# Performance work log

Hardware: AMD Instinct MI355X
Metric: run time of the kernel (lower is better)

The kernel has to match this reference:

```python
import jax, jax.numpy as jnp
import numpy as np

B, N, DIN, H, A = 4096, 32, 256, 128, 32  # batch, n_agents, din, hidden_dim, n_actions
NEG = 9e15


def _linear_params(key, fan_in, fan_out):
    kw, kb = jax.random.split(key)
    bound = 1.0 / np.sqrt(fan_in)
    w = jax.random.uniform(kw, (fan_in, fan_out), jnp.float32, -bound, bound)
    b = jax.random.uniform(kb, (fan_out,), jnp.float32, -bound, bound)
    return w, b


def setup_inputs() -> dict:
    key = jax.random.key(0)
    ks = jax.random.split(key, 12)
    x = jax.random.normal(ks[0], (B, N, DIN), jnp.float32)
    mask = jax.random.randint(ks[1], (B, N, N), 0, 2).astype(jnp.float32)
    enc_w, enc_b = _linear_params(ks[2], DIN, H)
    a1_vw, a1_vb = _linear_params(ks[3], H, H)
    a1_kw, a1_kb = _linear_params(ks[4], H, H)
    a1_qw, a1_qb = _linear_params(ks[5], H, H)
    a1_ow, a1_ob = _linear_params(ks[6], H, H)
    a2_vw, a2_vb = _linear_params(ks[7], H, H)
    a2_kw, a2_kb = _linear_params(ks[8], H, H)
    a2_qw, a2_qb = _linear_params(ks[9], H, H)
    a2_ow, a2_ob = _linear_params(ks[10], H, H)
    q_w, q_b = _linear_params(ks[11], H, A)
    return dict(x=x, mask=mask, enc_w=enc_w, enc_b=enc_b,
                a1_vw=a1_vw, a1_vb=a1_vb, a1_kw=a1_kw, a1_kb=a1_kb,
                a1_qw=a1_qw, a1_qb=a1_qb, a1_ow=a1_ow, a1_ob=a1_ob,
                a2_vw=a2_vw, a2_vb=a2_vb, a2_kw=a2_kw, a2_kb=a2_kb,
                a2_qw=a2_qw, a2_qb=a2_qb, a2_ow=a2_ow, a2_ob=a2_ob,
                q_w=q_w, q_b=q_b)


def _att_block(h, mask, vw, vb, kw, kb, qw, qb, ow, ob):
    # h: [B, N, H]; mask: [B, N, N]
    v = jax.nn.relu(jnp.einsum('bnd,dh->bnh', h, vw) + vb)
    q = jax.nn.relu(jnp.einsum('bnd,dh->bnh', h, qw) + qb)
    k = jax.nn.relu(jnp.einsum('bnd,dh->bnh', h, kw) + kb)
    scores = jnp.einsum('bih,bjh->bij', q, k)               # [B, N, N]
    logits = scores * mask - NEG * (1.0 - mask)
    att = jax.nn.softmax(logits, axis=2)
    out = jnp.einsum('bij,bjh->bih', att, v)
    return jax.nn.relu(jnp.einsum('bnh,ho->bno', out, ow) + ob)


def reference(x, mask, enc_w, enc_b,
              a1_vw, a1_vb, a1_kw, a1_kb, a1_qw, a1_qb, a1_ow, a1_ob,
              a2_vw, a2_vb, a2_kw, a2_kb, a2_qw, a2_qb, a2_ow, a2_ob,
              q_w, q_b):
    h1 = jax.nn.relu(jnp.einsum('bnd,dh->bnh', x, enc_w) + enc_b)
    h2 = _att_block(h1, mask, a1_vw, a1_vb, a1_kw, a1_kb, a1_qw, a1_qb, a1_ow, a1_ob)
    h3 = _att_block(h2, mask, a2_vw, a2_vb, a2_kw, a2_kb, a2_qw, a2_qb, a2_ow, a2_ob)
    q = jnp.einsum('bnh,ha->bna', h3, q_w) + q_b            # [B, N, A]
    return q
```

## Files before the change

kernel.cpp:

```cpp
#include <hip/hip_runtime.h>
#include <hip/hip_bf16.h>

typedef __attribute__((ext_vector_type(8))) short bf16x8;
typedef __attribute__((ext_vector_type(4))) short bf16x4;
typedef __attribute__((ext_vector_type(4))) float f32x4;

#define DEVI static __device__ __forceinline__

constexpr int NAG = 32, DIN = 256, HDIM = 128, ADIM = 32;

constexpr int WS_ENC = 0;
constexpr int WS_H   = 32768;
constexpr int WS_QW  = 32768 + 8 * 16384;
constexpr int WS_TOT = WS_QW + 4096;

constexpr int SH = 136;
constexpr int SV = 40;
constexpr int SA = 40;
constexpr int SX = 264;

constexpr int L_P0 = 0;
constexpr int L_P1 = 8704;
constexpr int L_P2 = 17408;
constexpr int L_PV = 26112;
constexpr int L_TOT = 36352;

DEVI short f2bf(float f) {
  union { float f; unsigned u; } a; a.f = f;
  return (short)((a.u + 0x7fffu + ((a.u >> 16) & 1u)) >> 16);
}

__global__ void prep_weights(const float* __restrict__ enc_w,
                             const float* __restrict__ m0, const float* __restrict__ m1,
                             const float* __restrict__ m2, const float* __restrict__ m3,
                             const float* __restrict__ m4, const float* __restrict__ m5,
                             const float* __restrict__ m6, const float* __restrict__ m7,
                             const float* __restrict__ qw,
                             short* __restrict__ ws)
{
  const int blk = blockIdx.x, tid = threadIdx.x;
  const float* src; int base, NM, nsh, f4;
  if (blk < 32) { src = enc_w; base = WS_ENC; NM = 8; nsh = 7; f4 = blk * 256 + tid; }
  else if (blk < 160) {
    const int m = (blk - 32) >> 4;
    if      (m == 0) src = m0; else if (m == 1) src = m1;
    else if (m == 2) src = m2; else if (m == 3) src = m3;
    else if (m == 4) src = m4; else if (m == 5) src = m5;
    else if (m == 6) src = m6; else             src = m7;
    base = WS_H + (m << 14); NM = 8; nsh = 7; f4 = ((blk - 32) & 15) * 256 + tid;
  } else { src = qw; base = WS_QW; NM = 2; nsh = 5; f4 = (blk - 160) * 256 + tid; }
  const int s = f4 * 4;
  const int row = s >> nsh, col0 = s & ((1 << nsh) - 1);
  const float4 v = *(const float4*)(src + s);
  const int j = row & 7, ks = row >> 5, lhi = ((row >> 3) & 3) * 16;
  const float vv[4] = {v.x, v.y, v.z, v.w};
#pragma unroll
  for (int c = 0; c < 4; ++c) {
    const int col = col0 + c;
    const int mt = col >> 4, lane = lhi + (col & 15);
    ws[base + (((ks * NM + mt) * 64 + lane) << 3) + j] = f2bf(vv[c]);
  }
}

template<int KSTEPS, bool RELU>
DEVI void linearSw4(const short* __restrict__ src, int sstride,
                    const short* __restrict__ wfrag, const float* __restrict__ bias,
                    short* __restrict__ dst,
                    int mg, int lr, int lq, int lane)
{
  f32x4 acc[2][2];
#pragma unroll
  for (int a = 0; a < 2; ++a)
#pragma unroll
    for (int b = 0; b < 2; ++b) acc[a][b] = (f32x4){0.f, 0.f, 0.f, 0.f};

  const bf16x8* wp = (const bf16x8*)wfrag;
#pragma unroll
  for (int ks = 0; ks < KSTEPS; ++ks) {
    bf16x8 hb[2];
#pragma unroll
    for (int b = 0; b < 2; ++b)
      hb[b] = *(const bf16x8*)(src + (b * 16 + lr) * sstride + ks * 32 + lq * 8);
#pragma unroll
    for (int a = 0; a < 2; ++a) {
      const bf16x8 wa = wp[(ks * 8 + mg * 2 + a) * 64 + lane];
#pragma unroll
      for (int b = 0; b < 2; ++b)
        acc[a][b] = __builtin_amdgcn_mfma_f32_16x16x32_bf16(wa, hb[b], acc[a][b], 0, 0, 0);
    }
  }
#pragma unroll
  for (int a = 0; a < 2; ++a) {
    const float4 bv = *(const float4*)(bias + (mg * 2 + a) * 16 + lq * 4);
    const float bb[4] = {bv.x, bv.y, bv.z, bv.w};
#pragma unroll
    for (int b = 0; b < 2; ++b) {
      bf16x4 s;
#pragma unroll
      for (int r = 0; r < 4; ++r) {
        float v = acc[a][b][r] + bb[r];
        if (RELU) v = fmaxf(v, 0.f);
        s[r] = f2bf(v);
      }
      *(bf16x4*)(dst + (b * 16 + lr) * SH + (mg * 2 + a) * 16 + lq * 4) = s;
    }
  }
}

DEVI void qkv_pass4(const short* __restrict__ h,
                    const short* __restrict__ wq, const short* __restrict__ wk,
                    const short* __restrict__ wv,
                    const float* __restrict__ bq, const float* __restrict__ bk,
                    const float* __restrict__ bv,
                    short* __restrict__ Q, short* __restrict__ K, short* __restrict__ V,
                    int mg, int lr, int lq, int lane)
{
  f32x4 qa[2][2], ka[2][2], va[2][2];
#pragma unroll
  for (int a = 0; a < 2; ++a)
#pragma unroll
    for (int b = 0; b < 2; ++b) {
      qa[a][b] = (f32x4){0.f, 0.f, 0.f, 0.f};
      ka[a][b] = (f32x4){0.f, 0.f, 0.f, 0.f};
      va[a][b] = (f32x4){0.f, 0.f, 0.f, 0.f};
    }
  const bf16x8* wpq = (const bf16x8*)wq;
  const bf16x8* wpk = (const bf16x8*)wk;
  const bf16x8* wpv = (const bf16x8*)wv;
#pragma unroll
  for (int ks = 0; ks < 4; ++ks) {
    bf16x8 hf[2];
#pragma unroll
    for (int b = 0; b < 2; ++b)
      hf[b] = *(const bf16x8*)(h + (b * 16 + lr) * SH + ks * 32 + lq * 8);
#pragma unroll
    for (int a = 0; a < 2; ++a) {
      const bf16x8 wqf = wpq[(ks * 8 + mg * 2 + a) * 64 + lane];
      const bf16x8 wkf = wpk[(ks * 8 + mg * 2 + a) * 64 + lane];
      const bf16x8 wvf = wpv[(ks * 8 + mg * 2 + a) * 64 + lane];
#pragma unroll
      for (int b = 0; b < 2; ++b) {
        qa[a][b] = __builtin_amdgcn_mfma_f32_16x16x32_bf16(wqf, hf[b], qa[a][b], 0, 0, 0);
        ka[a][b] = __builtin_amdgcn_mfma_f32_16x16x32_bf16(wkf, hf[b], ka[a][b], 0, 0, 0);
        va[b][a] = __builtin_amdgcn_mfma_f32_16x16x32_bf16(hf[b], wvf, va[b][a], 0, 0, 0);
      }
    }
  }
#pragma unroll
  for (int a = 0; a < 2; ++a) {
    const float4 bq4 = *(const float4*)(bq + (mg * 2 + a) * 16 + lq * 4);
    const float4 bk4 = *(const float4*)(bk + (mg * 2 + a) * 16 + lq * 4);
    const float qb4[4] = {bq4.x, bq4.y, bq4.z, bq4.w};
    const float kb4[4] = {bk4.x, bk4.y, bk4.z, bk4.w};
#pragma unroll
    for (int b = 0; b < 2; ++b) {
      bf16x4 sq, sk;
#pragma unroll
      for (int r = 0; r < 4; ++r) {
        sq[r] = f2bf(fmaxf(qa[a][b][r] + qb4[r], 0.f));
        sk[r] = f2bf(fmaxf(ka[a][b][r] + kb4[r], 0.f));
      }
      const int off = (b * 16 + lr) * SH + (mg * 2 + a) * 16 + lq * 4;
      *(bf16x4*)(Q + off) = sq;
      *(bf16x4*)(K + off) = sk;
    }
  }
#pragma unroll
  for (int a = 0; a < 2; ++a) {
    const float bvv = bv[(mg * 2 + a) * 16 + lr];
#pragma unroll
    for (int b = 0; b < 2; ++b) {
      bf16x4 sv;
#pragma unroll
      for (int r = 0; r < 4; ++r)
        sv[r] = f2bf(fmaxf(va[b][a][r] + bvv, 0.f));
      *(bf16x4*)(V + ((mg * 2 + a) * 16 + lr) * SV + b * 16 + lq * 4) = sv;
    }
  }
}

DEVI void scores_pass4(const short* __restrict__ Q, const short* __restrict__ K,
                       short* __restrict__ AT, const float* __restrict__ mask,
                       int b0, int qt, int lr, int lq)
{
  f32x4 sc[2];
  sc[0] = (f32x4){0.f, 0.f, 0.f, 0.f};
  sc[1] = (f32x4){0.f, 0.f, 0.f, 0.f};
#pragma unroll
  for (int ks = 0; ks < 4; ++ks) {
    const bf16x8 qf = *(const bf16x8*)(Q + (qt * 16 + lr) * SH + ks * 32 + lq * 8);
#pragma unroll
    for (int kt = 0; kt < 2; ++kt) {
      const bf16x8 kf = *(const bf16x8*)(K + (kt * 16 + lr) * SH + ks * 32 + lq * 8);
      sc[kt] = __builtin_amdgcn_mfma_f32_16x16x32_bf16(kf, qf, sc[kt], 0, 0, 0);
    }
  }
  const float* mp = mask + (size_t)b0 * (NAG * NAG) + (qt * 16 + lr) * 32;
  float l[2][4];
  float M = -3.0e38f;
#pragma unroll
  for (int kt = 0; kt < 2; ++kt) {
    const float4 m4 = *(const float4*)(mp + kt * 16 + lq * 4);
    const float mm[4] = {m4.x, m4.y, m4.z, m4.w};
#pragma unroll
    for (int r = 0; r < 4; ++r) {
      const float v = sc[kt][r] * mm[r] - 9e15f * (1.f - mm[r]);
      l[kt][r] = v;
      M = fmaxf(M, v);
    }
  }
  M = fmaxf(M, __shfl_xor(M, 16));
  M = fmaxf(M, __shfl_xor(M, 32));
  float e[2][4], T = 0.f;
#pragma unroll
  for (int kt = 0; kt < 2; ++kt)
#pragma unroll
    for (int r = 0; r < 4; ++r) { e[kt][r] = __expf(l[kt][r] - M); T += e[kt][r]; }
  T += __shfl_xor(T, 16);
  T += __shfl_xor(T, 32);
  const float rT = __frcp_rn(T);
#pragma unroll
  for (int kt = 0; kt < 2; ++kt) {
    bf16x4 s;
#pragma unroll
    for (int r = 0; r < 4; ++r) s[r] = f2bf(e[kt][r] * rT);
    *(bf16x4*)(AT + (qt * 16 + lr) * SA + kt * 16 + lq * 4) = s;
  }
}

DEVI void pv_pass4(const short* __restrict__ V, const short* __restrict__ AT,
                   short* __restrict__ AO, int wave, int lr, int lq)
{
  bf16x8 atf[2];
#pragma unroll
  for (int qt = 0; qt < 2; ++qt)
    atf[qt] = *(const bf16x8*)(AT + (qt * 16 + lr) * SA + lq * 8);
#pragma unroll
  for (int fi = 0; fi < 2; ++fi) {
    const int f2 = wave * 2 + fi;
    const bf16x8 vf = *(const bf16x8*)(V + (f2 * 16 + lr) * SV + lq * 8);
#pragma unroll
    for (int qt = 0; qt < 2; ++qt) {
      const f32x4 p = __builtin_amdgcn_mfma_f32_16x16x32_bf16(
          vf, atf[qt], (f32x4){0.f, 0.f, 0.f, 0.f}, 0, 0, 0);
      bf16x4 s;
#pragma unroll
      for (int r = 0; r < 4; ++r) s[r] = f2bf(p[r]);
      *(bf16x4*)(AO + (qt * 16 + lr) * SH + f2 * 16 + lq * 4) = s;
    }
  }
}

DEVI void att_block4(const short* Rh, short* RQ, short* RK, short* RV,
                     short* RAT, short* RAO, short* Rout,
                     const short* wv, const short* wk, const short* wq, const short* wo,
                     const float* bv, const float* bk, const float* bq, const float* bo,
                     const float* __restrict__ mask, int b0,
                     int wave, int lr, int lq, int lane)
{
  qkv_pass4(Rh, wq, wk, wv, bq, bk, bv, RQ, RK, RV, wave, lr, lq, lane);
  __syncthreads();
  if (wave < 2) scores_pass4(RQ, RK, RAT, mask, b0, wave, lr, lq);
  __syncthreads();
  pv_pass4(RV, RAT, RAO, wave, lr, lq);
  __syncthreads();
  linearSw4<4, true>(RAO, SH, wo, bo, Rout, wave, lr, lq, lane);
  __syncthreads();
}

__global__ __launch_bounds__(256, 4)
void dgn_main(const float* __restrict__ x, const float* __restrict__ mask,
              const float* __restrict__ enc_b,
              const float* __restrict__ b1v, const float* __restrict__ b1k,
              const float* __restrict__ b1q, const float* __restrict__ b1o,
              const float* __restrict__ b2v, const float* __restrict__ b2k,
              const float* __restrict__ b2q, const float* __restrict__ b2o,
              const float* __restrict__ qb,
              const short* __restrict__ wf,
              float* __restrict__ out)
{
  __shared__ __align__(16) char smem[L_TOT];
  short* P0 = (short*)(smem + L_P0);
  short* P1 = (short*)(smem + L_P1);
  short* P2 = (short*)(smem + L_P2);
  short* PV = (short*)(smem + L_PV);
  short* XB = (short*)(smem + L_P1);

  const int tid = threadIdx.x;
  const int wave = tid >> 6, lane = tid & 63;
  const int lr = lane & 15, lq = lane >> 4;
  const int b0 = blockIdx.x;

  {
    const float4* xsrc = (const float4*)(x + (size_t)b0 * NAG * DIN);
#pragma unroll
    for (int it = 0; it < 8; ++it) {
      const int q4 = tid + it * 256;
      const float4 v = xsrc[q4];
      bf16x4 s;
      s[0] = f2bf(v.x); s[1] = f2bf(v.y); s[2] = f2bf(v.z); s[3] = f2bf(v.w);
      *(bf16x4*)(XB + (q4 >> 6) * SX + (q4 & 63) * 4) = s;
    }
  }
  __syncthreads();

  linearSw4<8, true>(XB, SX, wf + WS_ENC, enc_b, P0, wave, lr, lq, lane);
  __syncthreads();

  att_block4(P0, P1, P2, PV, P0, P1, P2,
             wf + WS_H + 0 * 16384, wf + WS_H + 1 * 16384,
             wf + WS_H + 2 * 16384, wf + WS_H + 3 * 16384,
             b1v, b1k, b1q, b1o, mask, b0, wave, lr, lq, lane);

  att_block4(P2, P0, P1, PV, P2, P0, P1,
             wf + WS_H + 4 * 16384, wf + WS_H + 5 * 16384,
             wf + WS_H + 6 * 16384, wf + WS_H + 7 * 16384,
             b2v, b2k, b2q, b2o, mask, b0, wave, lr, lq, lane);

  if (wave < 2) {
    f32x4 ha[2];
    ha[0] = (f32x4){0.f, 0.f, 0.f, 0.f};
    ha[1] = (f32x4){0.f, 0.f, 0.f, 0.f};
    const bf16x8* wp = (const bf16x8*)(wf + WS_QW);
#pragma unroll
    for (int ks = 0; ks < 4; ++ks) {
      const bf16x8 hf = *(const bf16x8*)(P1 + (wave * 16 + lr) * SH + ks * 32 + lq * 8);
#pragma unroll
      for (int a = 0; a < 2; ++a)
        ha[a] = __builtin_amdgcn_mfma_f32_16x16x32_bf16(wp[(ks * 2 + a) * 64 + lane], hf, ha[a], 0, 0, 0);
    }
    float* op = out + ((size_t)b0 * NAG + wave * 16 + lr) * ADIM;
#pragma unroll
    for (int a = 0; a < 2; ++a) {
      const float4 bv4 = *(const float4*)(qb + a * 16 + lq * 4);
      float4 o;
      o.x = ha[a][0] + bv4.x; o.y = ha[a][1] + bv4.y;
      o.z = ha[a][2] + bv4.z; o.w = ha[a][3] + bv4.w;
      *(float4*)(op + a * 16 + lq * 4) = o;
    }
  }
}

extern "C" void kernel_launch(void* const* d_in, const int* in_sizes, int n_in,
                              void* d_out, int out_size, void* d_ws, size_t ws_size,
                              hipStream_t stream)
{
  const float* x     = (const float*)d_in[0];
  const float* mask  = (const float*)d_in[1];
  const float* enc_w = (const float*)d_in[2];
  const float* enc_b = (const float*)d_in[3];
  const float* a1_vw = (const float*)d_in[4];
  const float* a1_vb = (const float*)d_in[5];
  const float* a1_kw = (const float*)d_in[6];
  const float* a1_kb = (const float*)d_in[7];
  const float* a1_qw = (const float*)d_in[8];
  const float* a1_qb = (const float*)d_in[9];
  const float* a1_ow = (const float*)d_in[10];
  const float* a1_ob = (const float*)d_in[11];
  const float* a2_vw = (const float*)d_in[12];
  const float* a2_vb = (const float*)d_in[13];
  const float* a2_kw = (const float*)d_in[14];
  const float* a2_kb = (const float*)d_in[15];
  const float* a2_qw = (const float*)d_in[16];
  const float* a2_qb = (const float*)d_in[17];
  const float* a2_ow = (const float*)d_in[18];
  const float* a2_ob = (const float*)d_in[19];
  const float* q_w   = (const float*)d_in[20];
  const float* q_b   = (const float*)d_in[21];
  short* ws = (short*)d_ws;

  prep_weights<<<164, 256, 0, stream>>>(
      enc_w, a1_vw, a1_kw, a1_qw, a1_ow, a2_vw, a2_kw, a2_qw, a2_ow, q_w, ws);

  dgn_main<<<4096, 256, 0, stream>>>(
      x, mask, enc_b,
      a1_vb, a1_kb, a1_qb, a1_ob,
      a2_vb, a2_kb, a2_qb, a2_ob,
      q_b, ws, (float*)d_out);
}
```

Baseline: 291.8 us.

## Swizzle LDS layouts, shrink shared memory, prefetch mask, split final linear across waves

New measurement: 387.4 us. 1.33x slower.

```diff
diff --git a/kernel.cpp b/kernel.cpp
--- a/kernel.cpp
+++ b/kernel.cpp
@@ -12,18 +12,16 @@
 constexpr int WS_ENC = 0;
 constexpr int WS_H   = 32768;
 constexpr int WS_QW  = 32768 + 8 * 16384;
-constexpr int WS_TOT = WS_QW + 4096;
-
-constexpr int SH = 136;
-constexpr int SV = 40;
-constexpr int SA = 40;
-constexpr int SX = 264;
-
-constexpr int L_P0 = 0;
-constexpr int L_P1 = 8704;
-constexpr int L_P2 = 17408;
-constexpr int L_PV = 26112;
-constexpr int L_TOT = 36352;
+
+constexpr int L_P0 = 0, L_P1 = 8192, L_P2 = 16384, L_PV = 24576, L_TOT = 32768;
+
+template<int ROWB>
+DEVI int offR(int row, int bcol) {
+  return row * ROWB + (((bcol >> 4) ^ (row & 15)) << 4) + (bcol & 15);
+}
+DEVI int offVA(int row, int bcol) {
+  return row * 64 + (((bcol >> 4) ^ ((row >> 1) & 3)) << 4) + (bcol & 15);
+}
 
 DEVI short f2bf(float f) {
   union { float f; unsigned u; } a; a.f = f;
@@ -62,10 +60,10 @@
   }
 }
 
-template<int KSTEPS, bool RELU>
-DEVI void linearSw4(const short* __restrict__ src, int sstride,
+template<int KSTEPS, bool RELU, int SRB>
+DEVI void linearSw4(const char* __restrict__ src,
                     const short* __restrict__ wfrag, const float* __restrict__ bias,
-                    short* __restrict__ dst,
+                    char* __restrict__ dst,
                     int mg, int lr, int lq, int lane)
 {
   f32x4 acc[2][2];
@@ -80,7 +78,7 @@
     bf16x8 hb[2];
 #pragma unroll
     for (int b = 0; b < 2; ++b)
-      hb[b] = *(const bf16x8*)(src + (b * 16 + lr) * sstride + ks * 32 + lq * 8);
+      hb[b] = *(const bf16x8*)(src + offR<SRB>(b * 16 + lr, ks * 64 + lq * 16));
 #pragma unroll
     for (int a = 0; a < 2; ++a) {
       const bf16x8 wa = wp[(ks * 8 + mg * 2 + a) * 64 + lane];
@@ -102,17 +100,17 @@
         if (RELU) v = fmaxf(v, 0.f);
         s[r] = f2bf(v);
       }
-      *(bf16x4*)(dst + (b * 16 + lr) * SH + (mg * 2 + a) * 16 + lq * 4) = s;
-    }
-  }
-}
-
-DEVI void qkv_pass4(const short* __restrict__ h,
+      *(bf16x4*)(dst + offR<256>(b * 16 + lr, (mg * 2 + a) * 32 + lq * 8)) = s;
+    }
+  }
+}
+
+DEVI void qkv_pass4(const char* __restrict__ h,
                     const short* __restrict__ wq, const short* __restrict__ wk,
                     const short* __restrict__ wv,
                     const float* __restrict__ bq, const float* __restrict__ bk,
                     const float* __restrict__ bv,
-                    short* __restrict__ Q, short* __restrict__ K, short* __restrict__ V,
+                    char* __restrict__ Q, char* __restrict__ K, char* __restrict__ V,
                     int mg, int lr, int lq, int lane)
 {
   f32x4 qa[2][2], ka[2][2], va[2][2];
@@ -132,7 +130,7 @@
     bf16x8 hf[2];
 #pragma unroll
     for (int b = 0; b < 2; ++b)
-      hf[b] = *(const bf16x8*)(h + (b * 16 + lr) * SH + ks * 32 + lq * 8);
+      hf[b] = *(const bf16x8*)(h + offR<256>(b * 16 + lr, ks * 64 + lq * 16));
 #pragma unroll
     for (int a = 0; a < 2; ++a) {
       const bf16x8 wqf = wpq[(ks * 8 + mg * 2 + a) * 64 + lane];
@@ -160,7 +158,7 @@
         sq[r] = f2bf(fmaxf(qa[a][b][r] + qb4[r], 0.f));
         sk[r] = f2bf(fmaxf(ka[a][b][r] + kb4[r], 0.f));
       }
-      const int off = (b * 16 + lr) * SH + (mg * 2 + a) * 16 + lq * 4;
+      const int off = offR<256>(b * 16 + lr, (mg * 2 + a) * 32 + lq * 8);
       *(bf16x4*)(Q + off) = sq;
       *(bf16x4*)(K + off) = sk;
     }
@@ -174,41 +172,39 @@
 #pragma unroll
       for (int r = 0; r < 4; ++r)
         sv[r] = f2bf(fmaxf(va[b][a][r] + bvv, 0.f));
-      *(bf16x4*)(V + ((mg * 2 + a) * 16 + lr) * SV + b * 16 + lq * 4) = sv;
-    }
-  }
-}
-
-DEVI void scores_pass4(const short* __restrict__ Q, const short* __restrict__ K,
-                       short* __restrict__ AT, const float* __restrict__ mask,
-                       int b0, int qt, int lr, int lq)
+      *(bf16x4*)(V + offVA((mg * 2 + a) * 16 + lr, b * 32 + lq * 8)) = sv;
+    }
+  }
+}
+
+DEVI void scores_pass4(const char* __restrict__ Q, const char* __restrict__ K,
+                       char* __restrict__ AT,
+                       float4 m40, float4 m41, int qt, int lr, int lq)
 {
   f32x4 sc[2];
   sc[0] = (f32x4){0.f, 0.f, 0.f, 0.f};
   sc[1] = (f32x4){0.f, 0.f, 0.f, 0.f};
 #pragma unroll
   for (int ks = 0; ks < 4; ++ks) {
-    const bf16x8 qf = *(const bf16x8*)(Q + (qt * 16 + lr) * SH + ks * 32 + lq * 8);
+    const bf16x8 qf = *(const bf16x8*)(Q + offR<256>(qt * 16 + lr, ks * 64 + lq * 16));
 #pragma unroll
     for (int kt = 0; kt < 2; ++kt) {
-      const bf16x8 kf = *(const bf16x8*)(K + (kt * 16 + lr) * SH + ks * 32 + lq * 8);
+      const bf16x8 kf = *(const bf16x8*)(K + offR<256>(kt * 16 + lr, ks * 64 + lq * 16));
       sc[kt] = __builtin_amdgcn_mfma_f32_16x16x32_bf16(kf, qf, sc[kt], 0, 0, 0);
     }
   }
-  const float* mp = mask + (size_t)b0 * (NAG * NAG) + (qt * 16 + lr) * 32;
+  const float mm[2][4] = {{m40.x, m40.y, m40.z, m40.w},
+                          {m41.x, m41.y, m41.z, m41.w}};
   float l[2][4];
   float M = -3.0e38f;
 #pragma unroll
-  for (int kt = 0; kt < 2; ++kt) {
-    const float4 m4 = *(const float4*)(mp + kt * 16 + lq * 4);
-    const float mm[4] = {m4.x, m4.y, m4.z, m4.w};
+  for (int kt = 0; kt < 2; ++kt)
 #pragma unroll
     for (int r = 0; r < 4; ++r) {
-      const float v = sc[kt][r] * mm[r] - 9e15f * (1.f - mm[r]);
+      const float v = (mm[kt][r] != 0.0f) ? sc[kt][r] : -9.0e15f;
       l[kt][r] = v;
       M = fmaxf(M, v);
     }
-  }
   M = fmaxf(M, __shfl_xor(M, 16));
   M = fmaxf(M, __shfl_xor(M, 32));
   float e[2][4], T = 0.f;
@@ -224,21 +220,21 @@
     bf16x4 s;
 #pragma unroll
     for (int r = 0; r < 4; ++r) s[r] = f2bf(e[kt][r] * rT);
-    *(bf16x4*)(AT + (qt * 16 + lr) * SA + kt * 16 + lq * 4) = s;
-  }
-}
-
-DEVI void pv_pass4(const short* __restrict__ V, const short* __restrict__ AT,
-                   short* __restrict__ AO, int wave, int lr, int lq)
+    *(bf16x4*)(AT + offVA(qt * 16 + lr, kt * 32 + lq * 8)) = s;
+  }
+}
+
+DEVI void pv_pass4(const char* __restrict__ V, const char* __restrict__ AT,
+                   char* __restrict__ AO, int wave, int lr, int lq)
 {
   bf16x8 atf[2];
 #pragma unroll
   for (int qt = 0; qt < 2; ++qt)
-    atf[qt] = *(const bf16x8*)(AT + (qt * 16 + lr) * SA + lq * 8);
+    atf[qt] = *(const bf16x8*)(AT + offVA(qt * 16 + lr, lq * 16));
 #pragma unroll
   for (int fi = 0; fi < 2; ++fi) {
     const int f2 = wave * 2 + fi;
-    const bf16x8 vf = *(const bf16x8*)(V + (f2 * 16 + lr) * SV + lq * 8);
+    const bf16x8 vf = *(const bf16x8*)(V + offVA(f2 * 16 + lr, lq * 16));
 #pragma unroll
     for (int qt = 0; qt < 2; ++qt) {
       const f32x4 p = __builtin_amdgcn_mfma_f32_16x16x32_bf16(
@@ -246,29 +242,29 @@
       bf16x4 s;
 #pragma unroll
       for (int r = 0; r < 4; ++r) s[r] = f2bf(p[r]);
-      *(bf16x4*)(AO + (qt * 16 + lr) * SH + f2 * 16 + lq * 4) = s;
-    }
-  }
-}
-
-DEVI void att_block4(const short* Rh, short* RQ, short* RK, short* RV,
-                     short* RAT, short* RAO, short* Rout,
+      *(bf16x4*)(AO + offR<256>(qt * 16 + lr, f2 * 32 + lq * 8)) = s;
+    }
+  }
+}
+
+DEVI void att_block4(const char* Rh, char* RQ, char* RK, char* RV,
+                     char* RAT, char* RAO, char* Rout,
                      const short* wv, const short* wk, const short* wq, const short* wo,
                      const float* bv, const float* bk, const float* bq, const float* bo,
-                     const float* __restrict__ mask, int b0,
+                     float4 m0, float4 m1,
                      int wave, int lr, int lq, int lane)
 {
   qkv_pass4(Rh, wq, wk, wv, bq, bk, bv, RQ, RK, RV, wave, lr, lq, lane);
   __syncthreads();
-  if (wave < 2) scores_pass4(RQ, RK, RAT, mask, b0, wave, lr, lq);
+  if (wave < 2) scores_pass4(RQ, RK, RAT, m0, m1, wave, lr, lq);
   __syncthreads();
   pv_pass4(RV, RAT, RAO, wave, lr, lq);
   __syncthreads();
-  linearSw4<4, true>(RAO, SH, wo, bo, Rout, wave, lr, lq, lane);
-  __syncthreads();
-}
-
-__global__ __launch_bounds__(256, 4)
+  linearSw4<4, true, 256>(RAO, wo, bo, Rout, wave, lr, lq, lane);
+  __syncthreads();
+}
+
+__global__ __launch_bounds__(256, 5)
 void dgn_main(const float* __restrict__ x, const float* __restrict__ mask,
               const float* __restrict__ enc_b,
               const float* __restrict__ b1v, const float* __restrict__ b1k,
@@ -280,16 +276,23 @@
               float* __restrict__ out)
 {
   __shared__ __align__(16) char smem[L_TOT];
-  short* P0 = (short*)(smem + L_P0);
-  short* P1 = (short*)(smem + L_P1);
-  short* P2 = (short*)(smem + L_P2);
-  short* PV = (short*)(smem + L_PV);
-  short* XB = (short*)(smem + L_P1);
+  char* P0 = smem + L_P0;
+  char* P1 = smem + L_P1;
+  char* P2 = smem + L_P2;
+  char* PV = smem + L_PV;
+  char* XB = smem + L_P1;
 
   const int tid = threadIdx.x;
   const int wave = tid >> 6, lane = tid & 63;
   const int lr = lane & 15, lq = lane >> 4;
   const int b0 = blockIdx.x;
+
+  float4 m0 = (float4){0.f, 0.f, 0.f, 0.f}, m1 = m0;
+  if (wave < 2) {
+    const float* mp = mask + (size_t)b0 * (NAG * NAG) + (wave * 16 + lr) * 32 + lq * 4;
+    m0 = *(const float4*)(mp);
+    m1 = *(const float4*)(mp + 16);
+  }
 
   {
     const float4* xsrc = (const float4*)(x + (size_t)b0 * NAG * DIN);
@@ -299,45 +302,39 @@
       const float4 v = xsrc[q4];
       bf16x4 s;
       s[0] = f2bf(v.x); s[1] = f2bf(v.y); s[2] = f2bf(v.z); s[3] = f2bf(v.w);
-      *(bf16x4*)(XB + (q4 >> 6) * SX + (q4 & 63) * 4) = s;
-    }
-  }
-  __syncthreads();
-
-  linearSw4<8, true>(XB, SX, wf + WS_ENC, enc_b, P0, wave, lr, lq, lane);
+      *(bf16x4*)(XB + offR<512>(q4 >> 6, (q4 & 63) * 8)) = s;
+    }
+  }
+  __syncthreads();
+
+  linearSw4<8, true, 512>(XB, wf + WS_ENC, enc_b, P0, wave, lr, lq, lane);
   __syncthreads();
 
   att_block4(P0, P1, P2, PV, P0, P1, P2,
              wf + WS_H + 0 * 16384, wf + WS_H + 1 * 16384,
              wf + WS_H + 2 * 16384, wf + WS_H + 3 * 16384,
-             b1v, b1k, b1q, b1o, mask, b0, wave, lr, lq, lane);
+             b1v, b1k, b1q, b1o, m0, m1, wave, lr, lq, lane);
 
   att_block4(P2, P0, P1, PV, P2, P0, P1,
              wf + WS_H + 4 * 16384, wf + WS_H + 5 * 16384,
              wf + WS_H + 6 * 16384, wf + WS_H + 7 * 16384,
-             b2v, b2k, b2q, b2o, mask, b0, wave, lr, lq, lane);
-
-  if (wave < 2) {
-    f32x4 ha[2];
-    ha[0] = (f32x4){0.f, 0.f, 0.f, 0.f};
-    ha[1] = (f32x4){0.f, 0.f, 0.f, 0.f};
+             b2v, b2k, b2q, b2o, m0, m1, wave, lr, lq, lane);
+
+  {
+    const int at = wave >> 1, agt = wave & 1;
+    f32x4 ha = (f32x4){0.f, 0.f, 0.f, 0.f};
     const bf16x8* wp = (const bf16x8*)(wf + WS_QW);
 #pragma unroll
     for (int ks = 0; ks < 4; ++ks) {
-      const bf16x8 hf = *(const bf16x8*)(P1 + (wave * 16 + lr) * SH + ks * 32 + lq * 8);
-#pragma unroll
-      for (int a = 0; a < 2; ++a)
-        ha[a] = __builtin_amdgcn_mfma_f32_16x16x32_bf16(wp[(ks * 2 + a) * 64 + lane], hf, ha[a], 0, 0, 0);
-    }
-    float* op = out + ((size_t)b0 * NAG + wave * 16 + lr) * ADIM;
-#pragma unroll
-    for (int a = 0; a < 2; ++a) {
-      const float4 bv4 = *(const float4*)(qb + a * 16 + lq * 4);
-      float4 o;
-      o.x = ha[a][0] + bv4.x; o.y = ha[a][1] + bv4.y;
-      o.z = ha[a][2] + bv4.z; o.w = ha[a][3] + bv4.w;
-      *(float4*)(op + a * 16 + lq * 4) = o;
-    }
+      const bf16x8 hf = *(const bf16x8*)(P1 + offR<256>(agt * 16 + lr, ks * 64 + lq * 16));
+      ha = __builtin_amdgcn_mfma_f32_16x16x32_bf16(wp[(ks * 2 + at) * 64 + lane], hf, ha, 0, 0, 0);
+    }
+    const float4 bv4 = *(const float4*)(qb + at * 16 + lq * 4);
+    float* op = out + ((size_t)b0 * NAG + agt * 16 + lr) * ADIM;
+    float4 o;
+    o.x = ha[0] + bv4.x; o.y = ha[1] + bv4.y;
+    o.z = ha[2] + bv4.z; o.w = ha[3] + bv4.w;
+    *(float4*)(op + at * 16 + lq * 4) = o;
   }
 }
 
```
